# Kernel tuning notes

Hardware: AMD Instinct MI355X
Metric: run time of the kernel (lower is better)

## Reference

```python
import jax, jax.numpy as jnp
import numpy as np

B, N = 2, 2048
TOP_K = 48
NUM_RBF = 16
MAX_REL = 32            # max_relative_feature
NUM_POS = 16            # num_positional_embeddings
EDGE_FEATURES = 128
EDGE_IN = NUM_POS + NUM_RBF * 25  # 416
POS_IN = 2 * MAX_REL + 2          # 66 one-hot classes


def setup_inputs() -> dict:
    key = jax.random.key(0)
    k0, k1, k2, k3 = jax.random.split(key, 4)
    X = jax.random.normal(k0, (B, N, 4, 3), dtype=jnp.float32) * 3.0
    mask = jnp.ones((B, N), dtype=jnp.float32)
    R_idx = jnp.arange(B * N, dtype=jnp.int32).reshape(B, N)
    chain_labels = jax.random.randint(k1, (B, N), 0, 4).astype(jnp.int32)
    W_pos = 0.05 * jax.random.normal(k2, (POS_IN, NUM_POS), dtype=jnp.float32)
    b_pos = jnp.zeros((NUM_POS,), dtype=jnp.float32)
    W_edge = 0.05 * jax.random.normal(k3, (EDGE_IN, EDGE_FEATURES), dtype=jnp.float32)
    b_edge = jnp.zeros((EDGE_FEATURES,), dtype=jnp.float32)
    return {"X": X, "mask": mask, "R_idx": R_idx, "chain_labels": chain_labels,
            "W_pos": W_pos, "b_pos": b_pos, "W_edge": W_edge, "b_edge": b_edge}


def _rbf(D):
    # D: [..., K] -> [..., K, NUM_RBF]
    mu = jnp.linspace(2.0, 22.0, NUM_RBF)        # D_min=2, D_max=22
    sigma = (22.0 - 2.0) / NUM_RBF               # 1.25
    return jnp.exp(-(((D[..., None] - mu) / sigma) ** 2))


def _pair_dist(A, Bc):
    # A, Bc: [B, N, 3] -> [B, N, N]
    return jnp.sqrt(jnp.sum((A[:, :, None, :] - Bc[:, None, :, :]) ** 2, axis=-1) + 1e-6)


def reference(X, mask, R_idx, chain_labels, W_pos, b_pos, W_edge, b_edge):
    # virtual Cbeta from backbone geometry
    b = X[:, :, 1, :] - X[:, :, 0, :]
    c = X[:, :, 2, :] - X[:, :, 1, :]
    a = jnp.cross(b, c, axis=-1)
    Cb = -0.58273431 * a + 0.56802827 * b - 0.54067466 * c + X[:, :, 1, :]
    Ca, Nat, Cat, Oat = X[:, :, 1, :], X[:, :, 0, :], X[:, :, 2, :], X[:, :, 3, :]

    # masked Ca-Ca distances + k nearest neighbors
    mask2 = mask[:, None, :] * mask[:, :, None]
    D = mask2 * _pair_dist(Ca, Ca)
    D_adjust = D + (1.0 - mask2) * jnp.max(D, axis=-1, keepdims=True)
    neg_D, E_idx = jax.lax.top_k(-D_adjust, min(TOP_K, N))  # smallest distances
    D_neighbors = -neg_D                                     # [B, N, K]

    rbfs = [_rbf(D_neighbors)]
    pairs = [(Nat, Nat), (Cat, Cat), (Oat, Oat), (Cb, Cb),
             (Ca, Nat), (Ca, Cat), (Ca, Oat), (Ca, Cb),
             (Nat, Cat), (Nat, Oat), (Nat, Cb), (Cb, Cat), (Cb, Oat), (Oat, Cat),
             (Nat, Ca), (Cat, Ca), (Oat, Ca), (Cb, Ca),
             (Cat, Nat), (Oat, Nat), (Cb, Nat), (Cat, Cb), (Oat, Cb), (Cat, Oat)]
    for A_, B_ in pairs:  # fixed structural set of 24 atom-pair types
        Dab = _pair_dist(A_, B_)                          # [B, N, N]
        Dn = jnp.take_along_axis(Dab, E_idx, axis=2)      # [B, N, K]
        rbfs.append(_rbf(Dn))
    RBF_all = jnp.concatenate(rbfs, axis=-1)              # [B, N, K, 25*NUM_RBF]

    # relative positional / chain features at the gathered neighbors
    offset = R_idx[:, :, None] - R_idx[:, None, :]
    offset = jnp.take_along_axis(offset, E_idx, axis=2)   # [B, N, K]
    d_chains = (chain_labels[:, :, None] == chain_labels[:, None, :]).astype(jnp.int32)
    E_chains = jnp.take_along_axis(d_chains, E_idx, axis=2)

    d = jnp.clip(offset + MAX_REL, 0, 2 * MAX_REL)
    d = d * E_chains + (1 - E_chains) * (2 * MAX_REL + 1)
    d_onehot = jax.nn.one_hot(d, POS_IN, dtype=jnp.float32)  # [B, N, K, 66]
    E_positional = d_onehot @ W_pos + b_pos                  # [B, N, K, 16]

    E = jnp.concatenate((E_positional, RBF_all), axis=-1)    # [B, N, K, 416]
    E = E @ W_edge + b_edge                                  # [B, N, K, 128]
    return E, E_idx
```

## Files before the change

### kernel.cpp

```cpp
#include <hip/hip_runtime.h>
#include <hip/hip_bf16.h>
#include <stdint.h>

#define BB   2
#define NN   2048
#define BN   (BB*NN)
#define KTOP 48
#define EIN  416
#define EF   128
#define LROW 424
#define SROW 132

typedef __attribute__((ext_vector_type(8))) short s8v;
typedef __attribute__((ext_vector_type(4))) float f32x4;
typedef __attribute__((ext_vector_type(4))) unsigned int u32x4;
typedef unsigned short u16;
typedef unsigned int u32;
typedef unsigned long long u64;

__device__ __constant__ int cPA[25] = {1,0,2,3,4,1,1,1,1,0,0,0,4,4,3,0,2,3,4,2,3,4,2,3,2};
__device__ __constant__ int cPB[25] = {1,0,2,3,4,0,2,3,4,2,3,4,2,3,2,1,1,1,1,0,0,0,4,4,3};

__device__ __forceinline__ u16 bf16u(float x) {
  __hip_bfloat16 h = __float2bfloat16(x);
  return *reinterpret_cast<u16*>(&h);
}
__device__ __forceinline__ u32 pack2(float lo, float hi) {
  return (u32)bf16u(lo) | ((u32)bf16u(hi) << 16);
}

__global__ __launch_bounds__(256) void prep_kernel(const float* __restrict__ X,
                                                   const float* __restrict__ W_edge,
                                                   float* __restrict__ atoms5p,
                                                   float* __restrict__ capack4,
                                                   u16* __restrict__ wtf) {
  int tid = blockIdx.x * 256 + threadIdx.x;
  if (tid < EIN * EF) {
    int k = tid >> 7, n = tid & 127;
    wtf[((size_t)(k >> 3)) * 1024 + n * 8 + (k & 7)] = bf16u(W_edge[tid]);
  } else if (tid < EIN * EF + BN) {
    int idx = tid - EIN * EF;
    const float* x = X + (size_t)idx * 12;
    float Nx = x[0], Ny = x[1], Nz = x[2];
    float Cax = x[3], Cay = x[4], Caz = x[5];
    float Cx = x[6], Cy = x[7], Cz = x[8];
    float Ox = x[9], Oy = x[10], Oz = x[11];
    float bx = Cax - Nx, by = Cay - Ny, bz = Caz - Nz;
    float cx = Cx - Cax, cy = Cy - Cay, cz = Cz - Caz;
    float ax = by * cz - bz * cy;
    float ay = bz * cx - bx * cz;
    float az = bx * cy - by * cx;
    float Cbx = -0.58273431f * ax + 0.56802827f * bx - 0.54067466f * cx + Cax;
    float Cby = -0.58273431f * ay + 0.56802827f * by - 0.54067466f * cy + Cay;
    float Cbz = -0.58273431f * az + 0.56802827f * bz - 0.54067466f * cz + Caz;
    f32x4* o = (f32x4*)(atoms5p + (size_t)idx * 20);
    o[0] = (f32x4){Nx, Ny, Nz, 0.f};
    o[1] = (f32x4){Cax, Cay, Caz, 0.f};
    o[2] = (f32x4){Cx, Cy, Cz, 0.f};
    o[3] = (f32x4){Ox, Oy, Oz, 0.f};
    o[4] = (f32x4){Cbx, Cby, Cbz, 0.f};
    *(f32x4*)(capack4 + (size_t)idx * 4) = (f32x4){Cax, Cay, Caz, 0.f};
  }
}

__device__ __forceinline__ u32 blockExclScan(u32 v, u32* scanw, int t) {
  int lane = t & 63, w = t >> 6;
  u32 inc = v;
#pragma unroll
  for (int off = 1; off < 64; off <<= 1) {
    u32 o = __shfl_up(inc, off);
    if (lane >= off) inc += o;
  }
  if (lane == 63) scanw[w] = inc;
  __syncthreads();
  u32 base = 0;
  for (int ww = 0; ww < w; ++ww) base += scanw[ww];
  __syncthreads();
  return base + inc - v;
}

template<int NB, bool CHKPREF>
__device__ __forceinline__ void radix_round(u32* hist, u32* scanw, u32* selinfo, int t,
                                            const u32* kv, u32 pref, int prefShift,
                                            int binShift, u32 binMask, u32 r) {
  const int PB = NB / 256;
#pragma unroll
  for (int q = 0; q < PB / 4; ++q)
    *(u32x4*)&hist[t * PB + q * 4] = (u32x4){0, 0, 0, 0};
  __syncthreads();
#pragma unroll
  for (int s = 0; s < 8; ++s) {
    bool ok = (!CHKPREF) || ((kv[s] >> prefShift) == pref);
    if (ok) atomicAdd(&hist[(kv[s] >> binShift) & binMask], 1u);
  }
  __syncthreads();
  u32 loc[PB];
  u32 sum = 0;
#pragma unroll
  for (int q = 0; q < PB / 4; ++q) {
    u32x4 lv = *(u32x4*)&hist[t * PB + q * 4];
    loc[q * 4 + 0] = lv.x; loc[q * 4 + 1] = lv.y;
    loc[q * 4 + 2] = lv.z; loc[q * 4 + 3] = lv.w;
    sum += lv.x + lv.y + lv.z + lv.w;
  }
  int lane = t & 63, w = t >> 6;
  u32 inc = sum;
#pragma unroll
  for (int off = 1; off < 64; off <<= 1) {
    u32 o = __shfl_up(inc, off);
    if (lane >= off) inc += o;
  }
  if (lane == 63) scanw[w] = inc;
  __syncthreads();
  u32 base = 0;
  for (int ww = 0; ww < w; ++ww) base += scanw[ww];
  u32 c = base + inc - sum;
#pragma unroll
  for (int q = 0; q < PB; ++q) {
    u32 nc = c + loc[q];
    if (c < r && r <= nc) { selinfo[0] = (u32)(t * PB + q); selinfo[1] = r - c; }
    c = nc;
  }
  __syncthreads();
}

__global__ __launch_bounds__(256) void topk_kernel(const float* __restrict__ capack4,
                                                   const float* __restrict__ mask,
                                                   float* __restrict__ dtop,
                                                   float* __restrict__ eidx_f) {
  __shared__ u32 hist[4096];
  __shared__ u32 scanw[4];
  __shared__ u32 selinfo[2];
  __shared__ float redf[4];
  __shared__ u64 win[64];

  int row = blockIdx.x;
  int b = row >> 11, i = row & (NN - 1);
  int t = threadIdx.x, lane = t & 63, w = t >> 6;
  const float* cab4 = capack4 + (size_t)b * NN * 4;
  const float* mrow = mask + (size_t)b * NN;
  f32x4 ci = *(const f32x4*)&cab4[(size_t)i * 4];
  float mi = mrow[i];
  f32x4 mk0 = *(const f32x4*)&mrow[t * 8];
  f32x4 mk1 = *(const f32x4*)&mrow[t * 8 + 4];

  float dvv[8], m2v[8];
  float lmax = 0.f;
#pragma unroll
  for (int s = 0; s < 8; ++s) {
    f32x4 cj = *(const f32x4*)&cab4[(size_t)(t * 8 + s) * 4];
    float dx = ci.x - cj.x, dy = ci.y - cj.y, dz = ci.z - cj.z;
    float d = sqrtf(dx * dx + dy * dy + dz * dz + 1e-6f);
    float mj = (s < 4) ? mk0[s] : mk1[s - 4];
    float m2 = mi * mj;
    float D = m2 * d;
    dvv[s] = D; m2v[s] = m2;
    lmax = fmaxf(lmax, D);
  }
#pragma unroll
  for (int off = 32; off >= 1; off >>= 1) lmax = fmaxf(lmax, __shfl_xor(lmax, off));
  if (lane == 0) redf[w] = lmax;
  __syncthreads();
  float rmax = fmaxf(fmaxf(redf[0], redf[1]), fmaxf(redf[2], redf[3]));

  u32 kv[8];
#pragma unroll
  for (int s = 0; s < 8; ++s)
    kv[s] = __float_as_uint(dvv[s] + (1.0f - m2v[s]) * rmax);

  u32 r = KTOP;
  radix_round<4096, false>(hist, scanw, selinfo, t, kv, 0, 0, 20, 0xFFFu, r);
  u32 sel1 = selinfo[0]; r = selinfo[1];
  radix_round<1024, true>(hist, scanw, selinfo, t, kv, sel1, 20, 10, 0x3FFu, r);
  u32 sel2 = selinfo[0]; r = selinfo[1];
  u32 pref12 = (sel1 << 10) | sel2;
  radix_round<1024, true>(hist, scanw, selinfo, t, kv, pref12, 10, 0, 0x3FFu, r);
  u32 sel3 = selinfo[0];
  u32 takeEq = selinfo[1];
  u32 T = (sel1 << 20) | (sel2 << 10) | sel3;

  u32 lcnt = 0, ecnt = 0;
#pragma unroll
  for (int s = 0; s < 8; ++s) { lcnt += (kv[s] < T); ecnt += (kv[s] == T); }
  u32 ebase = blockExclScan(ecnt, scanw, t);
  u32 taken = 0;
  if (ebase < takeEq) { u32 room = takeEq - ebase; taken = room < ecnt ? room : ecnt; }
  u32 wbase = blockExclScan(lcnt + taken, scanw, t);
  u32 slot = wbase, tleft = taken;
#pragma unroll
  for (int s = 0; s < 8; ++s) {
    u32 j = (u32)(t * 8 + s);
    if (kv[s] < T) {
      win[slot++] = ((u64)kv[s] << 32) | j;
    } else if (kv[s] == T && tleft) {
      win[slot++] = ((u64)kv[s] << 32) | j;
      tleft--;
    }
  }
  __syncthreads();

  if (w == 0) {
    u64 key = (lane < KTOP) ? win[lane] : ~0ull;
#pragma unroll
    for (int k = 2; k <= 64; k <<= 1) {
#pragma unroll
      for (int jj = k >> 1; jj >= 1; jj >>= 1) {
        u64 p = __shfl_xor(key, jj);
        bool lowerl = (lane & jj) == 0;
        bool asc = (lane & k) == 0;
        u64 mn = p < key ? p : key;
        u64 mx = p < key ? key : p;
        key = (lowerl == asc) ? mn : mx;
      }
    }
    if (lane < KTOP) {
      u32 j = (u32)(key & 0xffffffffu);
      eidx_f[row * KTOP + lane] = (float)j;
      dtop[row * KTOP + lane] = __uint_as_float((u32)(key >> 32));
    }
  }
}

__global__ __launch_bounds__(256, 4) void edge_kernel(const float* __restrict__ atoms5p,
                                                      const u16* __restrict__ wtf,
                                                      const float* __restrict__ eidx_f,
                                                      const float* __restrict__ dtop,
                                                      const int* __restrict__ Ridx,
                                                      const int* __restrict__ chains,
                                                      const float* __restrict__ Wpos,
                                                      const float* __restrict__ bpos,
                                                      const float* __restrict__ bedge,
                                                      float* __restrict__ Eout) {
  __shared__ __align__(16) u16 featsm[KTOP * LROW];
  __shared__ int jbuf[KTOP];

  int row = blockIdx.x;
  int b = row >> 11, i = row & (NN - 1);
  int t = threadIdx.x;

  if (t < KTOP) jbuf[t] = (int)eidx_f[row * KTOP + t];
  __syncthreads();

  const float* atomsB = atoms5p + (size_t)b * NN * 20;

#pragma unroll
  for (int q = 0; q < 5; ++q) {
    int e = t + q * 256;
    if (e < KTOP * 26) {
      int k = e / 26;
      int c = e - k * 26;
      int j = jbuf[k];
      u32 pk[8];
      if (c == 0) {
        int Ri = Ridx[b * NN + i], Rj = Ridx[b * NN + j];
        int same = (chains[b * NN + i] == chains[b * NN + j]);
        int off = Ri - Rj + 32;
        off = off < 0 ? 0 : (off > 64 ? 64 : off);
        int drow = same ? off : 65;
        const float* wr = Wpos + drow * 16;
#pragma unroll
        for (int h = 0; h < 4; ++h) {
          f32x4 wv = *(const f32x4*)&wr[h * 4];
          f32x4 bv = *(const f32x4*)&bpos[h * 4];
          pk[h * 2 + 0] = pack2(wv.x + bv.x, wv.y + bv.y);
          pk[h * 2 + 1] = pack2(wv.z + bv.z, wv.w + bv.w);
        }
      } else {
        float D;
        if (c == 1) {
          D = dtop[row * KTOP + k];
        } else {
          int p = c - 1;
          f32x4 I = *(const f32x4*)&atomsB[(size_t)i * 20 + cPA[p] * 4];
          f32x4 J = *(const f32x4*)&atomsB[(size_t)j * 20 + cPB[p] * 4];
          float dx = I.x - J.x, dy = I.y - J.y, dz = I.z - J.z;
          D = sqrtf(dx * dx + dy * dy + dz * dz + 1e-6f);
        }
        float Dc = fminf(D, 40.0f);
        float t0 = (Dc - 2.0f) * 0.8f;
        float v = __expf(-t0 * t0);
        float g = __expf(2.13333333f * t0 - 1.13777778f);
#pragma unroll
        for (int h = 0; h < 8; ++h) {
          float lo = v; v *= g; g *= 0.10273985f;
          float hi = v; v *= g; g *= 0.10273985f;
          pk[h] = pack2(lo, hi);
        }
      }
      u32x4* dst = (u32x4*)&featsm[k * LROW + c * 16];
      dst[0] = (u32x4){pk[0], pk[1], pk[2], pk[3]};
      dst[1] = (u32x4){pk[4], pk[5], pk[6], pk[7]};
    }
  }
  __syncthreads();

  int w = t >> 6, lane = t & 63;
  int lr = lane & 15, lg = lane >> 4;
  f32x4 acc[3][2] = {};
  for (int kc = 0; kc < 13; ++kc) {
    s8v afrag[3];
#pragma unroll
    for (int mt = 0; mt < 3; ++mt)
      afrag[mt] = *reinterpret_cast<const s8v*>(&featsm[(mt * 16 + lr) * LROW + kc * 32 + lg * 8]);
#pragma unroll
    for (int nt = 0; nt < 2; ++nt) {
      int col = w * 32 + nt * 16 + lr;
      s8v bfrag = *reinterpret_cast<const s8v*>(&wtf[(size_t)(kc * 4 + lg) * 1024 + col * 8]);
#pragma unroll
      for (int mt = 0; mt < 3; ++mt)
        acc[mt][nt] = __builtin_amdgcn_mfma_f32_16x16x32_bf16(afrag[mt], bfrag, acc[mt][nt], 0, 0, 0);
    }
  }
  __syncthreads();

  float* stage = (float*)featsm;
  float bias0 = bedge[w * 32 + lr];
  float bias1 = bedge[w * 32 + 16 + lr];
#pragma unroll
  for (int nt = 0; nt < 2; ++nt) {
    float bias = nt ? bias1 : bias0;
    int col = w * 32 + nt * 16 + lr;
#pragma unroll
    for (int mt = 0; mt < 3; ++mt) {
#pragma unroll
      for (int qq = 0; qq < 4; ++qq) {
        int m = mt * 16 + lg * 4 + qq;
        stage[m * SROW + col] = acc[mt][nt][qq] + bias;
      }
    }
  }
  __syncthreads();

  float* orow = Eout + (size_t)row * KTOP * EF;
#pragma unroll
  for (int q2 = 0; q2 < 6; ++q2) {
    int o = t * 4 + q2 * 1024;
    int m = o >> 7, col = o & 127;
    f32x4 vv = *(f32x4*)&stage[m * SROW + col];
    *(f32x4*)&orow[m * EF + col] = vv;
  }
}

extern "C" void kernel_launch(void* const* d_in, const int* in_sizes, int n_in,
                              void* d_out, int out_size, void* d_ws, size_t ws_size,
                              hipStream_t stream) {
  const float* X = (const float*)d_in[0];
  const float* mask = (const float*)d_in[1];
  const int* Ridx = (const int*)d_in[2];
  const int* chains = (const int*)d_in[3];
  const float* Wpos = (const float*)d_in[4];
  const float* bpos = (const float*)d_in[5];
  const float* Wedge = (const float*)d_in[6];
  const float* bedge = (const float*)d_in[7];

  float* Eout = (float*)d_out;
  float* EidxF = Eout + (size_t)BN * KTOP * EF;

  u16* wtf = (u16*)d_ws;
  float* atoms5p = (float*)((char*)d_ws + 53248 * 2);
  float* capack4 = atoms5p + (size_t)BN * 20;
  float* dtop = capack4 + (size_t)BN * 4;

  prep_kernel<<<(EIN * EF + BN + 255) / 256, 256, 0, stream>>>(X, Wedge, atoms5p, capack4, wtf);
  topk_kernel<<<BN, 256, 0, stream>>>(capack4, mask, dtop, EidxF);
  edge_kernel<<<BN, 256, 0, stream>>>(atoms5p, wtf, EidxF, dtop, Ridx, chains, Wpos, bpos, bedge, Eout);
}
```

Measured before the change: 96.44 us.

## Generate RBF A-fragments in registers inside MFMA loop instead of LDS feature tile

```diff
diff --git a/kernel.cpp b/kernel.cpp
--- a/kernel.cpp
+++ b/kernel.cpp
@@ -8,8 +8,6 @@
 #define KTOP 48
 #define EIN  416
 #define EF   128
-#define LROW 424
-#define SROW 132
 
 typedef __attribute__((ext_vector_type(8))) short s8v;
 typedef __attribute__((ext_vector_type(4))) float f32x4;
@@ -221,6 +219,24 @@
   }
 }
 
+__device__ __forceinline__ s8v rbf8(float D, float mu0) {
+  float Dc = fminf(D, 40.0f);
+  float t0 = (Dc - mu0) * 0.8f;
+  float v0 = __expf(-t0 * t0);
+  float g = __expf(fmaf(2.13333333f, t0, -1.13777778f));
+  const float C = 0.10273985f;
+  float v1 = v0 * g; g *= C;
+  float v2 = v1 * g; g *= C;
+  float v3 = v2 * g; g *= C;
+  float v4 = v3 * g; g *= C;
+  float v5 = v4 * g; g *= C;
+  float v6 = v5 * g; g *= C;
+  float v7 = v6 * g;
+  union { u32x4 u; s8v s; } cv;
+  cv.u = (u32x4){pack2(v0, v1), pack2(v2, v3), pack2(v4, v5), pack2(v6, v7)};
+  return cv.s;
+}
+
 __global__ __launch_bounds__(256, 4) void edge_kernel(const float* __restrict__ atoms5p,
                                                       const u16* __restrict__ wtf,
                                                       const float* __restrict__ eidx_f,
@@ -231,113 +247,108 @@
                                                       const float* __restrict__ bpos,
                                                       const float* __restrict__ bedge,
                                                       float* __restrict__ Eout) {
-  __shared__ __align__(16) u16 featsm[KTOP * LROW];
+  __shared__ float D_lds[KTOP][29];
+  __shared__ u32 pos_lds[KTOP][8];
+  __shared__ f32x4 aJ[KTOP][5];
+  __shared__ f32x4 aI[5];
   __shared__ int jbuf[KTOP];
 
   int row = blockIdx.x;
   int b = row >> 11, i = row & (NN - 1);
   int t = threadIdx.x;
-
-  if (t < KTOP) jbuf[t] = (int)eidx_f[row * KTOP + t];
-  __syncthreads();
-
   const float* atomsB = atoms5p + (size_t)b * NN * 20;
+
+  if (t < KTOP * 5) {
+    int k = t / 5, a = t - k * 5;
+    int j = (int)eidx_f[row * KTOP + k];
+    aJ[k][a] = *(const f32x4*)&atomsB[(size_t)j * 20 + a * 4];
+    if (a == 0) jbuf[k] = j;
+  } else if (t < KTOP * 5 + 5) {
+    int a = t - KTOP * 5;
+    aI[a] = *(const f32x4*)&atomsB[(size_t)i * 20 + a * 4];
+  }
+  if (t < KTOP) D_lds[t][0] = dtop[row * KTOP + t];
+  __syncthreads();
 
 #pragma unroll
   for (int q = 0; q < 5; ++q) {
     int e = t + q * 256;
-    if (e < KTOP * 26) {
-      int k = e / 26;
-      int c = e - k * 26;
+    if (e < 1152) {
+      int k = e / 24;
+      int p = e - k * 24 + 1;
+      f32x4 I = aI[cPA[p]];
+      f32x4 J = aJ[k][cPB[p]];
+      float dx = I.x - J.x, dy = I.y - J.y, dz = I.z - J.z;
+      D_lds[k][p] = __builtin_amdgcn_sqrtf(dx * dx + dy * dy + dz * dz + 1e-6f);
+    } else if (e < 1200) {
+      int k = e - 1152;
       int j = jbuf[k];
+      int Ri = Ridx[b * NN + i], Rj = Ridx[b * NN + j];
+      int same = (chains[b * NN + i] == chains[b * NN + j]);
+      int off = Ri - Rj + 32;
+      off = off < 0 ? 0 : (off > 64 ? 64 : off);
+      int drow = same ? off : 65;
+      const float* wr = Wpos + drow * 16;
       u32 pk[8];
-      if (c == 0) {
-        int Ri = Ridx[b * NN + i], Rj = Ridx[b * NN + j];
-        int same = (chains[b * NN + i] == chains[b * NN + j]);
-        int off = Ri - Rj + 32;
-        off = off < 0 ? 0 : (off > 64 ? 64 : off);
-        int drow = same ? off : 65;
-        const float* wr = Wpos + drow * 16;
-#pragma unroll
-        for (int h = 0; h < 4; ++h) {
-          f32x4 wv = *(const f32x4*)&wr[h * 4];
-          f32x4 bv = *(const f32x4*)&bpos[h * 4];
-          pk[h * 2 + 0] = pack2(wv.x + bv.x, wv.y + bv.y);
-          pk[h * 2 + 1] = pack2(wv.z + bv.z, wv.w + bv.w);
-        }
-      } else {
-        float D;
-        if (c == 1) {
-          D = dtop[row * KTOP + k];
-        } else {
-          int p = c - 1;
-          f32x4 I = *(const f32x4*)&atomsB[(size_t)i * 20 + cPA[p] * 4];
-          f32x4 J = *(const f32x4*)&atomsB[(size_t)j * 20 + cPB[p] * 4];
-          float dx = I.x - J.x, dy = I.y - J.y, dz = I.z - J.z;
-          D = sqrtf(dx * dx + dy * dy + dz * dz + 1e-6f);
-        }
-        float Dc = fminf(D, 40.0f);
-        float t0 = (Dc - 2.0f) * 0.8f;
-        float v = __expf(-t0 * t0);
-        float g = __expf(2.13333333f * t0 - 1.13777778f);
-#pragma unroll
-        for (int h = 0; h < 8; ++h) {
-          float lo = v; v *= g; g *= 0.10273985f;
-          float hi = v; v *= g; g *= 0.10273985f;
-          pk[h] = pack2(lo, hi);
-        }
+#pragma unroll
+      for (int h = 0; h < 4; ++h) {
+        f32x4 wv = *(const f32x4*)&wr[h * 4];
+        f32x4 bv = *(const f32x4*)&bpos[h * 4];
+        pk[h * 2 + 0] = pack2(wv.x + bv.x, wv.y + bv.y);
+        pk[h * 2 + 1] = pack2(wv.z + bv.z, wv.w + bv.w);
       }
-      u32x4* dst = (u32x4*)&featsm[k * LROW + c * 16];
-      dst[0] = (u32x4){pk[0], pk[1], pk[2], pk[3]};
-      dst[1] = (u32x4){pk[4], pk[5], pk[6], pk[7]};
+      *(u32x4*)&pos_lds[k][0] = (u32x4){pk[0], pk[1], pk[2], pk[3]};
+      *(u32x4*)&pos_lds[k][4] = (u32x4){pk[4], pk[5], pk[6], pk[7]};
     }
   }
   __syncthreads();
 
   int w = t >> 6, lane = t & 63;
   int lr = lane & 15, lg = lane >> 4;
+  int col0 = w * 32 + lr, col1 = col0 + 16;
+  const float MU8 = 12.6666667f;
   f32x4 acc[3][2] = {};
-  for (int kc = 0; kc < 13; ++kc) {
-    s8v afrag[3];
-#pragma unroll
-    for (int mt = 0; mt < 3; ++mt)
-      afrag[mt] = *reinterpret_cast<const s8v*>(&featsm[(mt * 16 + lr) * LROW + kc * 32 + lg * 8]);
-#pragma unroll
-    for (int nt = 0; nt < 2; ++nt) {
-      int col = w * 32 + nt * 16 + lr;
-      s8v bfrag = *reinterpret_cast<const s8v*>(&wtf[(size_t)(kc * 4 + lg) * 1024 + col * 8]);
-#pragma unroll
-      for (int mt = 0; mt < 3; ++mt)
-        acc[mt][nt] = __builtin_amdgcn_mfma_f32_16x16x32_bf16(afrag[mt], bfrag, acc[mt][nt], 0, 0, 0);
-    }
-  }
-  __syncthreads();
-
-  float* stage = (float*)featsm;
-  float bias0 = bedge[w * 32 + lr];
-  float bias1 = bedge[w * 32 + 16 + lr];
-#pragma unroll
-  for (int nt = 0; nt < 2; ++nt) {
-    float bias = nt ? bias1 : bias0;
-    int col = w * 32 + nt * 16 + lr;
+
+  {
+    s8v bf0 = *reinterpret_cast<const s8v*>(&wtf[(size_t)lg * 1024 + col0 * 8]);
+    s8v bf1 = *reinterpret_cast<const s8v*>(&wtf[(size_t)lg * 1024 + col1 * 8]);
 #pragma unroll
     for (int mt = 0; mt < 3; ++mt) {
-#pragma unroll
-      for (int qq = 0; qq < 4; ++qq) {
-        int m = mt * 16 + lg * 4 + qq;
-        stage[m * SROW + col] = acc[mt][nt][qq] + bias;
+      int m = mt * 16 + lr;
+      s8v af;
+      if (lg < 2) {
+        af = *reinterpret_cast<const s8v*>(&pos_lds[m][lg * 4]);
+      } else {
+        af = rbf8(D_lds[m][0], (lg == 2) ? 2.0f : MU8);
       }
-    }
-  }
-  __syncthreads();
-
+      acc[mt][0] = __builtin_amdgcn_mfma_f32_16x16x32_bf16(af, bf0, acc[mt][0], 0, 0, 0);
+      acc[mt][1] = __builtin_amdgcn_mfma_f32_16x16x32_bf16(af, bf1, acc[mt][1], 0, 0, 0);
+    }
+  }
+#pragma unroll
+  for (int kc = 1; kc < 13; ++kc) {
+    int p = 2 * kc - 1 + (lg >> 1);
+    float mu0 = (lg & 1) ? MU8 : 2.0f;
+    s8v bf0 = *reinterpret_cast<const s8v*>(&wtf[(size_t)(kc * 4 + lg) * 1024 + col0 * 8]);
+    s8v bf1 = *reinterpret_cast<const s8v*>(&wtf[(size_t)(kc * 4 + lg) * 1024 + col1 * 8]);
+#pragma unroll
+    for (int mt = 0; mt < 3; ++mt) {
+      s8v af = rbf8(D_lds[mt * 16 + lr][p], mu0);
+      acc[mt][0] = __builtin_amdgcn_mfma_f32_16x16x32_bf16(af, bf0, acc[mt][0], 0, 0, 0);
+      acc[mt][1] = __builtin_amdgcn_mfma_f32_16x16x32_bf16(af, bf1, acc[mt][1], 0, 0, 0);
+    }
+  }
+
+  float bias0 = bedge[col0], bias1 = bedge[col1];
   float* orow = Eout + (size_t)row * KTOP * EF;
 #pragma unroll
-  for (int q2 = 0; q2 < 6; ++q2) {
-    int o = t * 4 + q2 * 1024;
-    int m = o >> 7, col = o & 127;
-    f32x4 vv = *(f32x4*)&stage[m * SROW + col];
-    *(f32x4*)&orow[m * EF + col] = vv;
+  for (int mt = 0; mt < 3; ++mt) {
+#pragma unroll
+    for (int qq = 0; qq < 4; ++qq) {
+      int m = mt * 16 + lg * 4 + qq;
+      orow[m * EF + col0] = acc[mt][0][qq] + bias0;
+      orow[m * EF + col1] = acc[mt][1][qq] + bias1;
+    }
   }
 }
 
```

New measurement: 104.2 us. +8.0%, slower.
